# Kernel tuning notes

Hardware: AMD Instinct MI355X
Metric: run time of the kernel (lower is better)

## Reference

```python
import jax, jax.numpy as jnp
import numpy as np

N, F_IN, F_OUT, H = 4096, 128, 64, 8
NEG_SLOPE = 0.2

def leaky_relu(x):
    return jnp.where(x >= 0, x, NEG_SLOPE * x)

def setup_inputs() -> dict:
    key = jax.random.key(0)
    k = jax.random.split(key, 6)
    x = jax.random.normal(k[0], (N, F_IN), dtype=jnp.float32)
    conn = jax.random.uniform(k[1], (N, N)) < 0.1
    conn = conn | jnp.eye(N, dtype=bool)
    topology = jnp.where(conn, 0.0, -1e9).astype(jnp.float32)
    proj = jax.random.normal(k[2], (H, F_IN, F_OUT), dtype=jnp.float32) * (1.0 / np.sqrt(F_IN))
    score_src = jax.random.normal(k[3], (H, F_OUT), dtype=jnp.float32) * (1.0 / np.sqrt(F_OUT))
    score_dst = jax.random.normal(k[4], (H, F_OUT), dtype=jnp.float32) * (1.0 / np.sqrt(F_OUT))
    skip_w = jax.random.normal(k[5], (H * F_OUT, F_IN), dtype=jnp.float32) * (1.0 / np.sqrt(F_IN))
    return {"x": x, "topology": topology, "proj": proj,
            "score_src": score_src, "score_dst": score_dst, "skip_w": skip_w}

def reference(x, topology, proj, score_src, score_dst, skip_w):
    # dropout is identity at inference time
    # projected node features: [H, N, F_OUT]
    h = jnp.einsum('ni,hio->hno', x, proj)
    # additive attention scores (GAT): [H, N, 1] + [H, 1, N] -> [H, N, N]
    s_src = jnp.einsum('hno,ho->hn', h, score_src)
    s_dst = jnp.einsum('hno,ho->hn', h, score_dst)
    scores = leaky_relu(s_src[:, :, None] + s_dst[:, None, :])
    attn = jax.nn.softmax(scores + topology[None, :, :], axis=-1)  # [H, N, N]
    # aggregate neighbors, then transpose heads to [N, H, F_OUT]
    out = jnp.einsum('hij,hjo->iho', attn, h)
    # skip connection (F_OUT != F_IN -> projected skip)
    out = out + (x @ skip_w.T).reshape(N, H, F_OUT)
    # mean over heads (concat_heads=False), then LeakyReLU activation
    out = leaky_relu(jnp.mean(out, axis=1))  # [N, F_OUT]
    return out
```

## Files before the change

kernel.cpp:

```cpp
#include <hip/hip_runtime.h>
#include <hip/hip_bf16.h>

#define NN 4096
#define FIN 128
#define FOUT 64
#define NH 8
#define KS 4

typedef float f32x4 __attribute__((ext_vector_type(4)));
typedef _Float16 f16x8 __attribute__((ext_vector_type(8)));
typedef _Float16 h2 __attribute__((ext_vector_type(2)));
typedef unsigned long long u64;

static __device__ __forceinline__ h2 as_h2(unsigned u) { return __builtin_bit_cast(h2, u); }
static __device__ __forceinline__ unsigned as_u32(h2 v) { return __builtin_bit_cast(unsigned, v); }

__global__ __launch_bounds__(256) void maskwc_kernel(
    const float* __restrict__ topo, u64* __restrict__ mb,
    const float* __restrict__ proj, const float* __restrict__ score_src,
    const float* __restrict__ score_dst, const float* __restrict__ skip_w,
    float* __restrict__ Wc) {
    const int tid = threadIdx.x;
    if (blockIdx.x < 2048) {
        const int w = blockIdx.x * 4 + (tid >> 6);
        const int lane = tid & 63;
        size_t base = (size_t)w * 32;
#pragma unroll 4
        for (int it = 0; it < 32; ++it) {
            size_t u = base + it;
            float t = topo[u * 64 + lane];
            u64 b = __ballot(t > -0.5e9f);
            if (lane == 0) mb[u] = b;
        }
        return;
    }
    int idx = (blockIdx.x - 2048) * 256 + tid;
    if (idx >= FIN * 80) return;
    int i = idx / 80, c = idx % 80;
    float v = 0.f;
    if (c < 16) {
        int h = c & 7;
        const float* w = (c < 8 ? score_src : score_dst) + h * FOUT;
        const float* p = proj + (size_t)h * FIN * FOUT + (size_t)i * FOUT;
        for (int f = 0; f < FOUT; ++f) v += p[f] * w[f];
    } else {
        int f = c - 16;
        for (int h = 0; h < NH; ++h) v += skip_w[(size_t)(h * FOUT + f) * FIN + i];
        v *= 0.125f;
    }
    Wc[i * 80 + c] = v;
}

__global__ __launch_bounds__(256) void scores_kernel(
    const float* __restrict__ x, const float* __restrict__ Wc,
    float* __restrict__ skipm, _Float16* __restrict__ Eh, _Float16* __restrict__ Fh,
    unsigned* __restrict__ Cc, _Float16* __restrict__ xb) {
    __shared__ float wcs[FIN][80];
    __shared__ float xs[16][FIN + 5];
    const int n0 = blockIdx.x * 16;
    const int tid = threadIdx.x;
    for (int i = tid; i < FIN * 80 / 4; i += 256)
        ((float4*)&wcs[0][0])[i] = ((const float4*)Wc)[i];
    const float4* xsrc = (const float4*)(x + (size_t)n0 * FIN);
    for (int i = tid; i < 16 * FIN / 4; i += 256) {
        int r = i >> 5, c4 = i & 31;
        *(float4*)&xs[r][c4 * 4] = xsrc[i];
    }
    __syncthreads();
    const int r = tid & 15;
    const int g = tid >> 4;
    float acc[4];
    float sa = 0.f;
#pragma unroll
    for (int j = 0; j < 4; ++j) acc[j] = 0.f;
#pragma unroll 4
    for (int i = 0; i < FIN; ++i) {
        float xv = xs[r][i];
        float4 p = *(float4*)&wcs[i][16 + g * 4];
        float qv = wcs[i][g];
        acc[0] += xv * p.x; acc[1] += xv * p.y; acc[2] += xv * p.z; acc[3] += xv * p.w;
        sa += xv * qv;
    }
    int n = n0 + r;
#pragma unroll
    for (int j = 0; j < 4; ++j) skipm[(size_t)n * FOUT + g * 4 + j] = acc[j];
    if (g < 8) {
        _Float16 c1 = (_Float16)(expf(sa) * 0.125f);
        _Float16 c2 = (_Float16)(expf(0.2f * sa) * 0.125f);
        unsigned short u1 = __builtin_bit_cast(unsigned short, c1);
        unsigned short u2 = __builtin_bit_cast(unsigned short, c2);
        Cc[(size_t)g * NN + n] = ((unsigned)u2 << 16) | (unsigned)u1;
    } else {
        int h = g - 8;
        Eh[(size_t)h * NN + n] = (_Float16)expf(sa);
        Fh[(size_t)h * NN + n] = (_Float16)expf(0.2f * sa);
    }
    {
        int row = tid >> 4, col0 = (tid & 15) * 8;
        const float* src = &xs[row][col0];
        f16x8 b0;
#pragma unroll
        for (int j = 0; j < 8; ++j) b0[j] = (_Float16)src[j];
        *(f16x8*)(xb + (size_t)(n0 + row) * FIN + col0) = b0;
    }
}

__global__ __launch_bounds__(256) void vt_kernel(
    const float* __restrict__ proj, const _Float16* __restrict__ xb,
    _Float16* __restrict__ Vt) {
    __shared__ _Float16 pT[FOUT][FIN + 8];
    const int tid = threadIdx.x;
    const int h = blockIdx.x >> 6;
    const int ng = blockIdx.x & 63;
    for (int idx = tid; idx < FIN * FOUT; idx += 256) {
        int i = idx >> 6, f = idx & 63;
        pT[f][i] = (_Float16)proj[(size_t)h * FIN * FOUT + idx];
    }
    __syncthreads();
    const int wave = tid >> 6, lane = tid & 63, q = lane >> 4, li = lane & 15;
    const int nb = ng * 64 + wave * 16;
    f32x4 acc[4];
#pragma unroll
    for (int n = 0; n < 4; ++n) acc[n] = (f32x4){0.f, 0.f, 0.f, 0.f};
#pragma unroll
    for (int kt = 0; kt < 4; ++kt) {
        f16x8 bfrag = *(const f16x8*)(xb + (size_t)(nb + li) * FIN + kt * 32 + q * 8);
#pragma unroll
        for (int ft = 0; ft < 4; ++ft) {
            f16x8 afrag = *(const f16x8*)&pT[ft * 16 + li][kt * 32 + q * 8];
            acc[ft] = __builtin_amdgcn_mfma_f32_16x16x32_f16(afrag, bfrag, acc[ft], 0, 0, 0);
        }
    }
#pragma unroll
    for (int ft = 0; ft < 4; ++ft)
#pragma unroll
        for (int reg = 0; reg < 4; ++reg)
            Vt[((size_t)h * FOUT + ft * 16 + q * 4 + reg) * NN + nb + li] = (_Float16)acc[ft][reg];
}

__attribute__((amdgpu_waves_per_eu(4)))
__global__ __launch_bounds__(256) void attn_kernel(
    const u64* __restrict__ maskbits, const _Float16* __restrict__ Vtg,
    const _Float16* __restrict__ Ehg, const _Float16* __restrict__ Fhg,
    const unsigned* __restrict__ Ccg,
    __hip_bfloat16* __restrict__ accP, float* __restrict__ rsP) {
    __shared__ u64 maskS[4][32][18];
    __shared__ char vbuf[4][4096];
    const int tid = threadIdx.x;
    const int w = tid >> 6;
    const int lane = tid & 63, q = lane >> 4, li = lane & 15;
    const int qt = blockIdx.x >> 5;
    const int ks = (blockIdx.x >> 3) & 3;
    const int h  = blockIdx.x & 7;
    const int row0 = qt * 128 + w * 32;
    const int kb0 = ks * 1024;

    const int r_ = lane >> 2;
    const int sg = ((lane & 3) - (r_ >> 1)) & 3;
    const _Float16* gsrc = Vtg + ((size_t)h * FOUT + w * 16 + r_) * NN + kb0 + sg * 8;
    const int rdoff = li * 64 + ((q + (li >> 1)) & 3) * 16;
    const _Float16* ehp = Ehg + (size_t)h * NN + kb0 + q * 8;
    const _Float16* fhp = Fhg + (size_t)h * NN + kb0 + q * 8;

#define DMA_TILE(B, OFF) \
    __builtin_amdgcn_global_load_lds( \
        (const __attribute__((address_space(1))) void*)(gsrc + (OFF)), \
        (__attribute__((address_space(3))) void*)&vbuf[B][w * 1024], 16, 0, 0)

    {
#pragma unroll
        for (int j = 0; j < 8; ++j) {
            int t = lane + j * 64;
            maskS[w][t >> 4][t & 15] =
                maskbits[(size_t)(row0 + (t >> 4)) * 64 + ks * 16 + (t & 15)];
        }
    }
    uint4 e0 = *(const uint4*)(ehp);
    uint4 f0 = *(const uint4*)(fhp);
    uint4 e1, f1;
    DMA_TILE(0, 0);
    DMA_TILE(1, 32);

    h2 c1h[2], c2h[2];
#pragma unroll
    for (int rt = 0; rt < 2; ++rt) {
        unsigned cw = Ccg[(size_t)h * NN + row0 + rt * 16 + li];
        c1h[rt] = as_h2((cw << 16) | (cw & 0xffffu));
        c2h[rt] = as_h2((cw >> 16) | (cw & 0xffff0000u));
    }
    __syncthreads();

    f16x8 ones;
#pragma unroll
    for (int j = 0; j < 8; ++j) ones[j] = (_Float16)1.0f;

    f32x4 acc[2][4];
    f32x4 rsacc[2];
#pragma unroll
    for (int rt = 0; rt < 2; ++rt) {
#pragma unroll
        for (int n = 0; n < 4; ++n) acc[rt][n] = (f32x4){0.f, 0.f, 0.f, 0.f};
        rsacc[rt] = (f32x4){0.f, 0.f, 0.f, 0.f};
    }

    const u64* mp0 = &maskS[w][li][0];
    const u64* mp1 = &maskS[w][16 + li][0];
    u64 ma0 = mp0[0], ma1 = mp1[0];
    u64 mb0 = mp0[1], mb1 = mp1[1];

#define BODY(K2, EU, FU, EN, FN, MW0, MW1) do {                                               \
    EN = *(const uint4*)(ehp + ((K2) + 1) * 32);                                              \
    FN = *(const uint4*)(fhp + ((K2) + 1) * 32);                                              \
    asm volatile("" ::: "memory");                        \
    DMA_TILE(((K2) + 2) & 3, ((K2) + 2) * 32);                                                \
    asm volatile("s_waitcnt vmcnt(4)" ::: "memory");                                          \
    __builtin_amdgcn_s_barrier();                                                             \
    f16x8 vf_[4];                                                                             \
    _Pragma("unroll")                                                                         \
    for (int n = 0; n < 4; ++n)                                                               \
        vf_[n] = *(const f16x8*)&vbuf[K2][n * 1024 + rdoff];                                  \
    unsigned ew_[4] = {EU.x, EU.y, EU.z, EU.w};                                               \
    unsigned fw_[4] = {FU.x, FU.y, FU.z, FU.w};                                               \
    _Pragma("unroll")                                                                         \
    for (int rt = 0; rt < 2; ++rt) {                                                          \
        u64 mw_ = rt ? (MW1) : (MW0);                                                         \
        unsigned mm_ = (unsigned)(mw_ >> (((K2) & 1) * 32 + q * 8)) & 0xffu;                  \
        unsigned mlo_ = mm_ & 0xFu, mhi_ = mm_ >> 4;                                          \
        unsigned blo_ = (mlo_ | (mlo_ << 7) | (mlo_ << 14) | (mlo_ << 21)) & 0x01010101u;     \
        unsigned bhi_ = (mhi_ | (mhi_ << 7) | (mhi_ << 14) | (mhi_ << 21)) & 0x01010101u;     \
        blo_ = (blo_ << 8) - blo_;                                                            \
        bhi_ = (bhi_ << 8) - bhi_;                                                            \
        unsigned mk_[4] = {__builtin_amdgcn_perm(0u, blo_, 0x01010000u),                      \
                           __builtin_amdgcn_perm(0u, blo_, 0x03030202u),                      \
                           __builtin_amdgcn_perm(0u, bhi_, 0x01010000u),                      \
                           __builtin_amdgcn_perm(0u, bhi_, 0x03030202u)};                     \
        union { f16x8 v; unsigned u[4]; } pf_;                                                \
        _Pragma("unroll")                                                                     \
        for (int j2 = 0; j2 < 4; ++j2) {                                                      \
            h2 t_ = c1h[rt] * as_h2(ew_[j2]);                                                 \
            h2 u_ = c2h[rt] * as_h2(fw_[j2]);                                                 \
            h2 p_ = __builtin_elementwise_max(t_, u_);                                        \
            pf_.u[j2] = as_u32(p_) & mk_[j2];                                                 \
        }                                                                                     \
        rsacc[rt] = __builtin_amdgcn_mfma_f32_16x16x32_f16(pf_.v, ones, rsacc[rt], 0, 0, 0);  \
        _Pragma("unroll")                                                                     \
        for (int n = 0; n < 4; ++n)                                                           \
            acc[rt][n] = __builtin_amdgcn_mfma_f32_16x16x32_f16(pf_.v, vf_[n], acc[rt][n],    \
                                                                0, 0, 0);                     \
    }                                                                                         \
} while (0)

#pragma unroll 1
    for (int i = 0; i < 8; ++i) {
        u64 na0 = mp0[2], na1 = mp1[2];
        u64 nb0 = mp0[3], nb1 = mp1[3];
        BODY(0, e0, f0, e1, f1, ma0, ma1);
        BODY(1, e1, f1, e0, f0, ma0, ma1);
        BODY(2, e0, f0, e1, f1, mb0, mb1);
        BODY(3, e1, f1, e0, f0, mb0, mb1);
        ma0 = na0; ma1 = na1; mb0 = nb0; mb1 = nb1;
        mp0 += 2; mp1 += 2;
        gsrc += 128; ehp += 128; fhp += 128;
    }
#undef BODY
#undef DMA_TILE

    asm volatile("s_waitcnt vmcnt(0)" ::: "memory");

#pragma unroll
    for (int rt = 0; rt < 2; ++rt) {
        if (li == 0) {
#pragma unroll
            for (int reg = 0; reg < 4; ++reg)
                rsP[(size_t)(ks * NH + h) * NN + row0 + rt * 16 + q * 4 + reg] = rsacc[rt][reg];
        }
        __hip_bfloat16* ap = accP + ((size_t)(ks * NH + h) * NN + row0 + rt * 16) * 64;
#pragma unroll
        for (int n = 0; n < 4; ++n)
#pragma unroll
            for (int reg = 0; reg < 4; ++reg)
                ap[(q * 4 + reg) * 64 + n * 16 + li] = __float2bfloat16(acc[rt][n][reg]);
    }
}

__global__ __launch_bounds__(256) void combine_kernel(
    const __hip_bfloat16* __restrict__ accP, const float* __restrict__ rsP,
    float* __restrict__ out) {
    int idx = blockIdx.x * 256 + threadIdx.x;
    int row = idx >> 6, f = idx & 63;
    float s = 0.f;
#pragma unroll 1
    for (int h = 0; h < NH; ++h) {
        float a = 0.f, r = 0.f;
#pragma unroll
        for (int k = 0; k < KS; ++k) {
            a += __bfloat162float(accP[((size_t)(k * NH + h) * NN + row) * 64 + f]);
            r += rsP[(size_t)(k * NH + h) * NN + row];
        }
        s += a / r;
    }
    float v = s * 0.125f + out[idx];
    out[idx] = fmaxf(v, 0.2f * v);
}

extern "C" void kernel_launch(void* const* d_in, const int* in_sizes, int n_in,
                              void* d_out, int out_size, void* d_ws, size_t ws_size,
                              hipStream_t stream) {
    (void)in_sizes; (void)n_in; (void)out_size; (void)ws_size;
    const float* x         = (const float*)d_in[0];
    const float* topology  = (const float*)d_in[1];
    const float* proj      = (const float*)d_in[2];
    const float* score_src = (const float*)d_in[3];
    const float* score_dst = (const float*)d_in[4];
    const float* skip_w    = (const float*)d_in[5];
    float* out = (float*)d_out;

    char* ws = (char*)d_ws;
    _Float16* xb   = (_Float16*)ws;
    _Float16* Vt   = (_Float16*)(ws + 1048576);
    _Float16* Eh   = (_Float16*)(ws + 5242880);
    _Float16* Fh   = (_Float16*)(ws + 5308416);
    unsigned* Cc   = (unsigned*)(ws + 5373952);
    float* Wc      = (float*)(ws + 5505024);
    u64* maskbits  = (u64*)(ws + 5545984);
    float* rsP     = (float*)(ws + 7643136);
    __hip_bfloat16* accP = (__hip_bfloat16*)(ws + 8167424);
    float* skipm = out;

    maskwc_kernel<<<2088, 256, 0, stream>>>(topology, maskbits, proj, score_src,
                                            score_dst, skip_w, Wc);
    scores_kernel<<<256, 256, 0, stream>>>(x, Wc, skipm, Eh, Fh, Cc, xb);
    vt_kernel<<<512, 256, 0, stream>>>(proj, xb, Vt);
    attn_kernel<<<1024, 256, 0, stream>>>(maskbits, Vt, Eh, Fh, Cc, accP, rsP);
    combine_kernel<<<1024, 256, 0, stream>>>(accP, rsP, out);
}
```

Before: 171.9 us.

## Vectorize mask packing, double-chunk attention pipeline, vectorize combine kernel

The mask-packing kernel now loads float4 per lane and interleaves four ballots with bit spreading, so each wave handles four columns per load. The attention loop now processes two 32-key chunks per barrier, using a triple-buffered LDS ring with 8 KB stages, and raises wave priority around the MFMA compute. This halves the number of barriers and waitcnts. The combine kernel handles four features per thread with vector loads and stores and a single reciprocal, launched with a quarter of the blocks. The trade-off is more LDS per block (24 KB of buffers plus the mask) and higher register pressure, which may reduce occupancy. The bit-spread layout must also match what the attention kernel expects.

```diff
diff --git a/kernel.cpp b/kernel.cpp
--- a/kernel.cpp
+++ b/kernel.cpp
@@ -14,6 +14,14 @@
 
 static __device__ __forceinline__ h2 as_h2(unsigned u) { return __builtin_bit_cast(h2, u); }
 static __device__ __forceinline__ unsigned as_u32(h2 v) { return __builtin_bit_cast(unsigned, v); }
+
+static __device__ __forceinline__ u64 spread4(u64 x) {
+    x = (x | (x << 24)) & 0x000000FF000000FFull;
+    x = (x | (x << 12)) & 0x000F000F000F000Full;
+    x = (x | (x << 6))  & 0x0303030303030303ull;
+    x = (x | (x << 3))  & 0x1111111111111111ull;
+    return x;
+}
 
 __global__ __launch_bounds__(256) void maskwc_kernel(
     const float* __restrict__ topo, u64* __restrict__ mb,
@@ -22,15 +30,32 @@
     float* __restrict__ Wc) {
     const int tid = threadIdx.x;
     if (blockIdx.x < 2048) {
-        const int w = blockIdx.x * 4 + (tid >> 6);
+        const int wg = blockIdx.x * 4 + (tid >> 6);
         const int lane = tid & 63;
-        size_t base = (size_t)w * 32;
-#pragma unroll 4
-        for (int it = 0; it < 32; ++it) {
-            size_t u = base + it;
-            float t = topo[u * 64 + lane];
-            u64 b = __ballot(t > -0.5e9f);
-            if (lane == 0) mb[u] = b;
+        const size_t base = (size_t)wg * 32;
+        const float* tp = topo + base * 64 + lane * 4;
+#pragma unroll
+        for (int it = 0; it < 8; ++it) {
+            float4 v = *(const float4*)(tp + it * 256);
+            u64 b0 = __ballot(v.x > -0.5e9f);
+            u64 b1 = __ballot(v.y > -0.5e9f);
+            u64 b2 = __ballot(v.z > -0.5e9f);
+            u64 b3 = __ballot(v.w > -0.5e9f);
+            u64 wv[4];
+#pragma unroll
+            for (int g = 0; g < 4; ++g) {
+                u64 x0 = spread4((b0 >> (16 * g)) & 0xFFFFu);
+                u64 x1 = spread4((b1 >> (16 * g)) & 0xFFFFu);
+                u64 x2 = spread4((b2 >> (16 * g)) & 0xFFFFu);
+                u64 x3 = spread4((b3 >> (16 * g)) & 0xFFFFu);
+                wv[g] = x0 | (x1 << 1) | (x2 << 2) | (x3 << 3);
+            }
+            if (lane == 0) {
+                ulonglong2 s01; s01.x = wv[0]; s01.y = wv[1];
+                ulonglong2 s23; s23.x = wv[2]; s23.y = wv[3];
+                *(ulonglong2*)&mb[base + it * 4] = s01;
+                *(ulonglong2*)&mb[base + it * 4 + 2] = s23;
+            }
         }
         return;
     }
@@ -144,8 +169,8 @@
     const _Float16* __restrict__ Ehg, const _Float16* __restrict__ Fhg,
     const unsigned* __restrict__ Ccg,
     __hip_bfloat16* __restrict__ accP, float* __restrict__ rsP) {
-    __shared__ u64 maskS[4][32][18];
-    __shared__ char vbuf[4][4096];
+    __shared__ u64 maskS[4][32][16];
+    __shared__ char vbufB[24576];
     const int tid = threadIdx.x;
     const int w = tid >> 6;
     const int lane = tid & 63, q = lane >> 4, li = lane & 15;
@@ -162,10 +187,10 @@
     const _Float16* ehp = Ehg + (size_t)h * NN + kb0 + q * 8;
     const _Float16* fhp = Fhg + (size_t)h * NN + kb0 + q * 8;
 
-#define DMA_TILE(B, OFF) \
+#define DMA_TILE(BYTEOFF, OFF) \
     __builtin_amdgcn_global_load_lds( \
         (const __attribute__((address_space(1))) void*)(gsrc + (OFF)), \
-        (__attribute__((address_space(3))) void*)&vbuf[B][w * 1024], 16, 0, 0)
+        (__attribute__((address_space(3))) void*)&vbufB[(BYTEOFF) + w * 1024], 16, 0, 0)
 
     {
 #pragma unroll
@@ -175,11 +200,13 @@
                 maskbits[(size_t)(row0 + (t >> 4)) * 64 + ks * 16 + (t & 15)];
         }
     }
-    uint4 e0 = *(const uint4*)(ehp);
-    uint4 f0 = *(const uint4*)(fhp);
-    uint4 e1, f1;
+    uint4 eA0 = *(const uint4*)(ehp);
+    uint4 fA0 = *(const uint4*)(fhp);
+    uint4 eA1 = *(const uint4*)(ehp + 32);
+    uint4 fA1 = *(const uint4*)(fhp + 32);
+    uint4 eB0, fB0, eB1, fB1;
     DMA_TILE(0, 0);
-    DMA_TILE(1, 32);
+    DMA_TILE(4096, 32);
 
     h2 c1h[2], c2h[2];
 #pragma unroll
@@ -208,23 +235,17 @@
     u64 ma0 = mp0[0], ma1 = mp1[0];
     u64 mb0 = mp0[1], mb1 = mp1[1];
 
-#define BODY(K2, EU, FU, EN, FN, MW0, MW1) do {                                               \
-    EN = *(const uint4*)(ehp + ((K2) + 1) * 32);                                              \
-    FN = *(const uint4*)(fhp + ((K2) + 1) * 32);                                              \
-    asm volatile("" ::: "memory");                        \
-    DMA_TILE(((K2) + 2) & 3, ((K2) + 2) * 32);                                                \
-    asm volatile("s_waitcnt vmcnt(4)" ::: "memory");                                          \
-    __builtin_amdgcn_s_barrier();                                                             \
+#define CHUNK_COMPUTE(CBYTE, EU, FU, PAR, MW0, MW1) do {                                      \
     f16x8 vf_[4];                                                                             \
     _Pragma("unroll")                                                                         \
     for (int n = 0; n < 4; ++n)                                                               \
-        vf_[n] = *(const f16x8*)&vbuf[K2][n * 1024 + rdoff];                                  \
+        vf_[n] = *(const f16x8*)&vbufB[(CBYTE) + n * 1024 + rdoff];                           \
     unsigned ew_[4] = {EU.x, EU.y, EU.z, EU.w};                                               \
     unsigned fw_[4] = {FU.x, FU.y, FU.z, FU.w};                                               \
     _Pragma("unroll")                                                                         \
     for (int rt = 0; rt < 2; ++rt) {                                                          \
         u64 mw_ = rt ? (MW1) : (MW0);                                                         \
-        unsigned mm_ = (unsigned)(mw_ >> (((K2) & 1) * 32 + q * 8)) & 0xffu;                  \
+        unsigned mm_ = (unsigned)(mw_ >> ((PAR) * 32 + q * 8)) & 0xffu;                       \
         unsigned mlo_ = mm_ & 0xFu, mhi_ = mm_ >> 4;                                          \
         unsigned blo_ = (mlo_ | (mlo_ << 7) | (mlo_ << 14) | (mlo_ << 21)) & 0x01010101u;     \
         unsigned bhi_ = (mhi_ | (mhi_ << 7) | (mhi_ << 14) | (mhi_ << 21)) & 0x01010101u;     \
@@ -250,21 +271,38 @@
     }                                                                                         \
 } while (0)
 
+#define SBODY(CB, DB, EU0, FU0, EU1, FU1, EN0, FN0, EN1, FN1, EO0, EO1, MW0, MW1) do {        \
+    EN0 = *(const uint4*)(ehp + (EO0));                                                       \
+    FN0 = *(const uint4*)(fhp + (EO0));                                                       \
+    EN1 = *(const uint4*)(ehp + (EO1));                                                       \
+    FN1 = *(const uint4*)(fhp + (EO1));                                                       \
+    asm volatile("" ::: "memory");                       \
+    DMA_TILE((DB), (EO0));                                                                    \
+    DMA_TILE((DB) + 4096, (EO1));                                                             \
+    asm volatile("s_waitcnt vmcnt(6)" ::: "memory");                                          \
+    __builtin_amdgcn_s_barrier();                                                             \
+    __builtin_amdgcn_s_setprio(1);                                                            \
+    CHUNK_COMPUTE((CB), EU0, FU0, 0, MW0, MW1);                                               \
+    CHUNK_COMPUTE((CB) + 4096, EU1, FU1, 1, MW0, MW1);                                        \
+    __builtin_amdgcn_s_setprio(0);                                                            \
+} while (0)
+
+    unsigned cb = 0, db = 8192;
 #pragma unroll 1
     for (int i = 0; i < 8; ++i) {
         u64 na0 = mp0[2], na1 = mp1[2];
         u64 nb0 = mp0[3], nb1 = mp1[3];
-        BODY(0, e0, f0, e1, f1, ma0, ma1);
-        BODY(1, e1, f1, e0, f0, ma0, ma1);
-        BODY(2, e0, f0, e1, f1, mb0, mb1);
-        BODY(3, e1, f1, e0, f0, mb0, mb1);
+        SBODY(cb, db, eA0, fA0, eA1, fA1, eB0, fB0, eB1, fB1, 64, 96, ma0, ma1);
+        cb = db; db += 8192; if (db == 24576) db = 0;
+        SBODY(cb, db, eB0, fB0, eB1, fB1, eA0, fA0, eA1, fA1, 128, 160, mb0, mb1);
+        cb = db; db += 8192; if (db == 24576) db = 0;
         ma0 = na0; ma1 = na1; mb0 = nb0; mb1 = nb1;
         mp0 += 2; mp1 += 2;
         gsrc += 128; ehp += 128; fhp += 128;
     }
-#undef BODY
+#undef SBODY
+#undef CHUNK_COMPUTE
 #undef DMA_TILE
-
     asm volatile("s_waitcnt vmcnt(0)" ::: "memory");
 
 #pragma unroll
@@ -287,20 +325,30 @@
     const __hip_bfloat16* __restrict__ accP, const float* __restrict__ rsP,
     float* __restrict__ out) {
     int idx = blockIdx.x * 256 + threadIdx.x;
-    int row = idx >> 6, f = idx & 63;
-    float s = 0.f;
+    int row = idx >> 4, fg = (idx & 15) * 4;
+    float s0 = 0.f, s1 = 0.f, s2 = 0.f, s3 = 0.f;
 #pragma unroll 1
     for (int h = 0; h < NH; ++h) {
-        float a = 0.f, r = 0.f;
+        float a0 = 0.f, a1 = 0.f, a2 = 0.f, a3 = 0.f, r = 0.f;
 #pragma unroll
         for (int k = 0; k < KS; ++k) {
-            a += __bfloat162float(accP[((size_t)(k * NH + h) * NN + row) * 64 + f]);
-            r += rsP[(size_t)(k * NH + h) * NN + row];
-        }
-        s += a / r;
-    }
-    float v = s * 0.125f + out[idx];
-    out[idx] = fmaxf(v, 0.2f * v);
+            const __hip_bfloat16* p = accP + ((size_t)(k * NH + h) * NN + row) * 64 + fg;
+            uint2 v = *(const uint2*)p;
+            a0 += __uint_as_float(v.x << 16);
+            a1 += __uint_as_float(v.x & 0xffff0000u);
+            a2 += __uint_as_float(v.y << 16);
+            a3 += __uint_as_float(v.y & 0xffff0000u);
+            r  += rsP[(size_t)(k * NH + h) * NN + row];
+        }
+        float ir = 1.0f / r;
+        s0 += a0 * ir; s1 += a1 * ir; s2 += a2 * ir; s3 += a3 * ir;
+    }
+    float4 o = *(float4*)(out + (size_t)row * 64 + fg);
+    float v0 = s0 * 0.125f + o.x, v1 = s1 * 0.125f + o.y;
+    float v2 = s2 * 0.125f + o.z, v3 = s3 * 0.125f + o.w;
+    o.x = fmaxf(v0, 0.2f * v0); o.y = fmaxf(v1, 0.2f * v1);
+    o.z = fmaxf(v2, 0.2f * v2); o.w = fmaxf(v3, 0.2f * v3);
+    *(float4*)(out + (size_t)row * 64 + fg) = o;
 }
 
 extern "C" void kernel_launch(void* const* d_in, const int* in_sizes, int n_in,
@@ -332,5 +380,5 @@
     scores_kernel<<<256, 256, 0, stream>>>(x, Wc, skipm, Eh, Fh, Cc, xb);
     vt_kernel<<<512, 256, 0, stream>>>(proj, xb, Vt);
     attn_kernel<<<1024, 256, 0, stream>>>(maskbits, Vt, Eh, Fh, Cc, accP, rsP);
-    combine_kernel<<<1024, 256, 0, stream>>>(accP, rsP, out);
-}
+    combine_kernel<<<256, 256, 0, stream>>>(accP, rsP, out);
+}
```

After: 187.5 us. 1.09x slower.
